# Kernel optimization log

Measured on AMD Instinct MI355X. Metric: run time of the kernel, lower is better.

The kernel has to match this reference:

```python
import jax, jax.numpy as jnp
import numpy as np

BATCH, SEQ, CH, ORDER = 4, 8192, 512, 64


def setup_inputs() -> dict:
    key = jax.random.key(0)
    k1, k2, k3 = jax.random.split(key, 3)
    x = jax.random.normal(k1, (BATCH, SEQ, CH), dtype=jnp.float32)
    # RTF parameters: small init so the denominator polynomial 1 + sum a_i z^-i
    # stays well-conditioned (stable transfer function), as in the FSSM init.
    A = 0.01 * jax.random.normal(k2, (CH, ORDER), dtype=jnp.float32)
    B = 0.01 * jax.random.normal(k3, (CH, ORDER), dtype=jnp.float32)
    h0 = jnp.zeros((1,), dtype=jnp.float32)
    return {"x": x, "A": A, "B": B, "h0": h0}


def _rtf_kernel(A, B, L):
    # Evaluate H(z) = b(z)/a(z) at the L roots of unity, then irfft -> impulse response.
    C = A.shape[0]
    a = jnp.concatenate([jnp.ones((C, 1), A.dtype), A], axis=-1)  # (C, N+1), leading coeff 1
    a_f = jnp.fft.rfft(a, n=L, axis=-1)                           # (C, L//2+1)
    b_f = jnp.fft.rfft(B, n=L, axis=-1)
    return jnp.fft.irfft(b_f / a_f, n=L, axis=-1)                 # (C, L)


def reference(x, A, B, h0):
    Bt, L, C = x.shape
    K = _rtf_kernel(A, B, L)                                      # (C, L)
    n_fft = 2 * L                                                 # causal (linear) convolution
    x_f = jnp.fft.rfft(x, n=n_fft, axis=1)                        # (B, n_fft//2+1, C)
    k_f = jnp.fft.rfft(K, n=n_fft, axis=-1).T[None]               # (1, n_fft//2+1, C)
    h1 = jnp.fft.irfft(x_f * k_f, n=n_fft, axis=1)[:, :L]         # (B, L, C)
    y1 = h1 + h0 * x
    return jax.nn.gelu(y1)
```

## Files before the change

### kernel.cpp

```cpp
#include <hip/hip_runtime.h>
#include <stdint.h>

#define NBATCH 4
#define LSEQ   8192
#define CH     512
#define ORDER  64
#define KTAP   256

typedef _Float16 half8 __attribute__((ext_vector_type(8)));
typedef _Float16 half4 __attribute__((ext_vector_type(4)));
typedef float    f32x4 __attribute__((ext_vector_type(4)));

#define PADP  8512
#define PAD0  279
#define NW    9

#define AFRAG_HALFS  ((size_t)CH * NW * 64 * 8)
#define XT_HALFS     ((size_t)CH * NBATCH * PADP)
#define WS_NEED      ((AFRAG_HALFS + XT_HALFS) * 2)

#define NAPREP 128
#define NXPOSE (133 * 8 * NBATCH)

__global__ __launch_bounds__(256) void prep(const float* __restrict__ A,
                                            const float* __restrict__ B,
                                            const float* __restrict__ h0,
                                            const float* __restrict__ x,
                                            _Float16* __restrict__ afr,
                                            _Float16* __restrict__ xT) {
    __shared__ float    Ksh[4][KTAP];
    __shared__ _Float16 tile[64][74];
    const int bid = blockIdx.x;
    if (bid < NAPREP) {
        const int wv = threadIdx.x >> 6, lane = threadIdx.x & 63;
        const int c  = bid * 4 + wv;
        const float a  = A[c * ORDER + lane];
        const float bc = B[c * ORDER + lane];
        const float h0v = h0[0];
        float s = 0.0f;
        for (int t = 0; t < KTAP; ++t) {
            const float s1 = __shfl(s, 0);
            const float bt = (t < ORDER) ? __shfl(bc, t) : 0.0f;
            const float y  = bt + s1;
            float su = __shfl_down(s, 1);
            if (lane == ORDER - 1) su = 0.0f;
            s = su - a * y;
            if (lane == 0) Ksh[wv][t] = (t == 0) ? (y + h0v) : y;
        }
        __syncthreads();
        const int i = lane & 15, g = lane >> 4;
        for (int w = 0; w < NW; ++w) {
            half8 hv;
#pragma unroll
            for (int e = 0; e < 8; ++e) {
                const int t = 32 * w + 15 + i - 8 * g - e;
                hv[e] = (_Float16)((t >= 0 && t < KTAP) ? Ksh[wv][t] : 0.0f);
            }
            *reinterpret_cast<half8*>(afr + ((size_t)(c * NW + w) * 64 + lane) * 8) = hv;
        }
    } else {
        const int bid2 = bid - NAPREP;
        const int px   = bid2 % 133;
        const int cy   = (bid2 / 133) & 7;
        const int bz   = bid2 / (133 * 8);
        const int p0 = px * 64, c0 = cy * 64, t = threadIdx.x;
        const int cl = (t & 15) * 4;
        const int rl = t >> 4;
#pragma unroll
        for (int pass = 0; pass < 4; ++pass) {
            const int pl = rl + 16 * pass;
            const int r  = p0 + pl - PAD0;
            float4 v = {0.0f, 0.0f, 0.0f, 0.0f};
            if (r >= 0 && r < LSEQ)
                v = *reinterpret_cast<const float4*>(x + ((size_t)bz * LSEQ + r) * CH + c0 + cl);
            tile[pl][cl + 0] = (_Float16)v.x;
            tile[pl][cl + 1] = (_Float16)v.y;
            tile[pl][cl + 2] = (_Float16)v.z;
            tile[pl][cl + 3] = (_Float16)v.w;
        }
        __syncthreads();
        const int pl2 = (t & 15) * 4;
#pragma unroll
        for (int pass = 0; pass < 4; ++pass) {
            const int cc = (t >> 4) + 16 * pass;
            half4 hv;
#pragma unroll
            for (int d = 0; d < 4; ++d) hv[d] = tile[pl2 + d][cc];
            *reinterpret_cast<half4*>(xT + ((size_t)((c0 + cc) * NBATCH + bz)) * PADP + p0 + pl2) = hv;
        }
    }
}

__global__ __launch_bounds__(256) void fir_mfma(const _Float16* __restrict__ xT,
                                                const _Float16* __restrict__ afr,
                                                float* __restrict__ out) {
    __shared__ _Float16 xs[16][1312];
    __shared__ float    lds_out[16][260];
    const int gid     = blockIdx.x;
    const int logical = (gid & 7) * 128 + (gid >> 3);
    const int chgrp   = logical >> 5;
    const int rem     = logical & 31;
    const int bb      = rem >> 3;
    const int tg      = rem & 7;

    {
        const int grp = threadIdx.x >> 4;
        const int l16 = threadIdx.x & 15;
        const size_t rowbase = ((size_t)(chgrp * 16 + grp) * NBATCH + bb) * PADP
                             + (size_t)tg * 1024 + 8;
#pragma unroll
        for (int it = 0; it < 11; ++it) {
            const int chunk = l16 + 16 * it;
            if (chunk < 164) {
                const half8 v = *reinterpret_cast<const half8*>(xT + rowbase + (size_t)chunk * 8);
                *reinterpret_cast<half8*>(&xs[grp][chunk * 8]) = v;
            }
        }
    }
    __syncthreads();

    const int wid = threadIdx.x >> 6, lane = threadIdx.x & 63;
    const int j = lane & 15, g = lane >> 4;
    const int c0 = chgrp * 16 + wid * 4;
    const _Float16* af = afr + (size_t)lane * 8;

    f32x4 acc[4][4];
#pragma unroll
    for (int ti = 0; ti < 4; ++ti)
#pragma unroll
        for (int q = 0; q < 4; ++q) acc[ti][q] = (f32x4){0.f, 0.f, 0.f, 0.f};

#pragma unroll
    for (int w = 0; w < NW; ++w) {
        half8 a[4];
#pragma unroll
        for (int q = 0; q < 4; ++q)
            a[q] = *reinterpret_cast<const half8*>(af + (size_t)((c0 + q) * NW + w) * 512);
        const int base = 16 * j + 8 * g - 32 * w + 256;
#pragma unroll
        for (int ti = 0; ti < 4; ++ti) {
#pragma unroll
            for (int q = 0; q < 4; ++q) {
                const half8 bv = *reinterpret_cast<const half8*>(&xs[wid * 4 + q][base + 256 * ti]);
                acc[ti][q] = __builtin_amdgcn_mfma_f32_16x16x32_f16(a[q], bv, acc[ti][q], 0, 0, 0);
            }
        }
    }

    const int ccs = threadIdx.x & 15, nb = threadIdx.x >> 4;
#pragma unroll
    for (int ti = 0; ti < 4; ++ti) {
        __syncthreads();
#pragma unroll
        for (int q = 0; q < 4; ++q) {
            f32x4 o;
#pragma unroll
            for (int r = 0; r < 4; ++r) {
                const float y  = acc[ti][q][r];
                const float m2 = y * y;
                const float wv = fmaf(m2, 0.14270963f, 1.5957691f);
                const float e  = __expf(y * wv);
                const float rc = __builtin_amdgcn_rcpf(e + 1.0f);
                o[r] = y - y * rc;
            }
            *reinterpret_cast<f32x4*>(&lds_out[wid * 4 + q][16 * j + 4 * g]) = o;
        }
        __syncthreads();
        const int n0 = tg * 1024 + ti * 256;
        float* ob = out + ((size_t)bb * LSEQ + n0) * CH + chgrp * 16 + ccs;
#pragma unroll
        for (int it = 0; it < 16; ++it) {
            const int nrel = nb + 16 * it;
            ob[(size_t)nrel * CH] = lds_out[ccs][nrel];
        }
    }
}

#define RINGF 32
#define CPBF  256
__global__ __launch_bounds__(ORDER) void rtf_impulse_fb(const float* __restrict__ A,
                                                        const float* __restrict__ B,
                                                        const float* __restrict__ h0,
                                                        float* __restrict__ kt4) {
    const int c = blockIdx.x, lane = threadIdx.x;
    const float a = A[c * ORDER + lane], bc = B[c * ORDER + lane], h0v = h0[0];
    float s = 0.0f;
    for (int t = 0; t < KTAP; ++t) {
        const float s1 = __shfl(s, 0);
        const float bt = (t < ORDER) ? __shfl(bc, t) : 0.0f;
        const float y  = bt + s1;
        float su = __shfl_down(s, 1);
        if (lane == ORDER - 1) su = 0.0f;
        s = su - a * y;
        if (lane == 0) kt4[((size_t)(t >> 2) * CH + c) * 4 + (t & 3)] = (t == 0) ? (y + h0v) : y;
    }
}
__global__ __launch_bounds__(CPBF) void fir_gelu_fb(const float* __restrict__ x,
                                                    const float* __restrict__ kt4,
                                                    float* __restrict__ out) {
    const int h = blockIdx.x;
    const int logical = ((h & 7) << 8) | (h >> 3);
    const int tile = logical & 255, sl = logical >> 8;
    const int cb = sl & 1, b = sl >> 1;
    const int c = cb * CPBF + threadIdx.x;
    const int n0 = tile * RINGF;
    const float* xb = x + (size_t)b * LSEQ * CH + c;
    const float4* kt4v = (const float4*)kt4;
    float acc[RINGF]; float ring[RINGF]; float px[2][8]; float kbuf[2][8];
#pragma unroll
    for (int r = 0; r < RINGF; ++r) acc[r] = 0.0f;
#pragma unroll
    for (int i = 0; i < RINGF; ++i) ring[i] = xb[(size_t)(n0 + i) * CH];
    {
        const float4 ka = kt4v[(size_t)0 * CH + c];
        const float4 kb = kt4v[(size_t)1 * CH + c];
        kbuf[0][0] = ka.x; kbuf[0][1] = ka.y; kbuf[0][2] = ka.z; kbuf[0][3] = ka.w;
        kbuf[0][4] = kb.x; kbuf[0][5] = kb.y; kbuf[0][6] = kb.z; kbuf[0][7] = kb.w;
#pragma unroll
        for (int g2 = 0; g2 < 8; ++g2) {
            const int m = n0 - 1 - g2;
            px[0][g2] = (m >= 0) ? xb[(size_t)m * CH] : 0.0f;
        }
    }
    for (int tb = 0; tb < KTAP; tb += RINGF) {
#pragma unroll
        for (int q = 0; q < 4; ++q) {
            const int cur = q & 1, nxt = cur ^ 1;
            const int tn = tb + 8 * (q + 1);
            if (tn < KTAP) {
                const float4 ka = kt4v[(size_t)(tn >> 2) * CH + c];
                const float4 kb = kt4v[(size_t)((tn >> 2) + 1) * CH + c];
                kbuf[nxt][0] = ka.x; kbuf[nxt][1] = ka.y; kbuf[nxt][2] = ka.z; kbuf[nxt][3] = ka.w;
                kbuf[nxt][4] = kb.x; kbuf[nxt][5] = kb.y; kbuf[nxt][6] = kb.z; kbuf[nxt][7] = kb.w;
#pragma unroll
                for (int g2 = 0; g2 < 8; ++g2) {
                    const int m = n0 - tn - 1 - g2;
                    px[nxt][g2] = (m >= 0) ? xb[(size_t)m * CH] : 0.0f;
                }
            }
#pragma unroll
            for (int g2 = 0; g2 < 8; ++g2) {
                const int tq = 8 * q + g2;
                const float kv = kbuf[cur][g2];
#pragma unroll
                for (int r = 0; r < RINGF; ++r)
                    acc[r] = fmaf(kv, ring[(r - tq) & (RINGF - 1)], acc[r]);
                ring[(RINGF - 1 - tq) & (RINGF - 1)] = px[cur][g2];
            }
        }
    }
    float* ob = out + ((size_t)b * LSEQ + n0) * CH + c;
#pragma unroll
    for (int r = 0; r < RINGF; ++r) {
        const float y = acc[r];
        const float m2 = y * y;
        const float wv = fmaf(m2, 0.14270963f, 1.5957691f);
        const float e = __expf(y * wv);
        const float rc = __builtin_amdgcn_rcpf(e + 1.0f);
        ob[(size_t)r * CH] = y - y * rc;
    }
}

extern "C" void kernel_launch(void* const* d_in, const int* in_sizes, int n_in,
                              void* d_out, int out_size, void* d_ws, size_t ws_size,
                              hipStream_t stream) {
    const float* x  = (const float*)d_in[0];
    const float* A  = (const float*)d_in[1];
    const float* B  = (const float*)d_in[2];
    const float* h0 = (const float*)d_in[3];
    float* out = (float*)d_out;

    if (ws_size >= WS_NEED) {
        _Float16* afr = (_Float16*)d_ws;
        _Float16* xT  = afr + AFRAG_HALFS;
        prep<<<dim3(NAPREP + NXPOSE), dim3(256), 0, stream>>>(A, B, h0, x, afr, xT);
        fir_mfma<<<dim3(1024), dim3(256), 0, stream>>>(xT, afr, out);
    } else {
        float* kt4 = (float*)d_ws;
        rtf_impulse_fb<<<dim3(CH), dim3(ORDER), 0, stream>>>(A, B, h0, kt4);
        fir_gelu_fb<<<dim3((LSEQ / RINGF) * (CH / CPBF) * NBATCH), dim3(CPBF), 0, stream>>>(x, kt4, out);
    }
}
```

Measured before the change: 60.74 us.

## Fuse x transpose/fp16 conversion into FIR kernel and vectorize output stores

```diff
diff --git a/kernel.cpp b/kernel.cpp
--- a/kernel.cpp
+++ b/kernel.cpp
@@ -8,112 +8,92 @@
 #define KTAP   256
 
 typedef _Float16 half8 __attribute__((ext_vector_type(8)));
-typedef _Float16 half4 __attribute__((ext_vector_type(4)));
+typedef _Float16 f16x2 __attribute__((ext_vector_type(2)));
 typedef float    f32x4 __attribute__((ext_vector_type(4)));
 
-#define PADP  8512
-#define PAD0  279
 #define NW    9
-
 #define AFRAG_HALFS  ((size_t)CH * NW * 64 * 8)
-#define XT_HALFS     ((size_t)CH * NBATCH * PADP)
-#define WS_NEED      ((AFRAG_HALFS + XT_HALFS) * 2)
-
-#define NAPREP 128
-#define NXPOSE (133 * 8 * NBATCH)
-
-__global__ __launch_bounds__(256) void prep(const float* __restrict__ A,
-                                            const float* __restrict__ B,
-                                            const float* __restrict__ h0,
-                                            const float* __restrict__ x,
-                                            _Float16* __restrict__ afr,
-                                            _Float16* __restrict__ xT) {
-    __shared__ float    Ksh[4][KTAP];
-    __shared__ _Float16 tile[64][74];
-    const int bid = blockIdx.x;
-    if (bid < NAPREP) {
-        const int wv = threadIdx.x >> 6, lane = threadIdx.x & 63;
-        const int c  = bid * 4 + wv;
-        const float a  = A[c * ORDER + lane];
-        const float bc = B[c * ORDER + lane];
-        const float h0v = h0[0];
-        float s = 0.0f;
-        for (int t = 0; t < KTAP; ++t) {
-            const float s1 = __shfl(s, 0);
-            const float bt = (t < ORDER) ? __shfl(bc, t) : 0.0f;
-            const float y  = bt + s1;
-            float su = __shfl_down(s, 1);
-            if (lane == ORDER - 1) su = 0.0f;
-            s = su - a * y;
-            if (lane == 0) Ksh[wv][t] = (t == 0) ? (y + h0v) : y;
-        }
-        __syncthreads();
-        const int i = lane & 15, g = lane >> 4;
-        for (int w = 0; w < NW; ++w) {
-            half8 hv;
-#pragma unroll
-            for (int e = 0; e < 8; ++e) {
-                const int t = 32 * w + 15 + i - 8 * g - e;
-                hv[e] = (_Float16)((t >= 0 && t < KTAP) ? Ksh[wv][t] : 0.0f);
-            }
-            *reinterpret_cast<half8*>(afr + ((size_t)(c * NW + w) * 64 + lane) * 8) = hv;
-        }
-    } else {
-        const int bid2 = bid - NAPREP;
-        const int px   = bid2 % 133;
-        const int cy   = (bid2 / 133) & 7;
-        const int bz   = bid2 / (133 * 8);
-        const int p0 = px * 64, c0 = cy * 64, t = threadIdx.x;
-        const int cl = (t & 15) * 4;
-        const int rl = t >> 4;
-#pragma unroll
-        for (int pass = 0; pass < 4; ++pass) {
-            const int pl = rl + 16 * pass;
-            const int r  = p0 + pl - PAD0;
-            float4 v = {0.0f, 0.0f, 0.0f, 0.0f};
-            if (r >= 0 && r < LSEQ)
-                v = *reinterpret_cast<const float4*>(x + ((size_t)bz * LSEQ + r) * CH + c0 + cl);
-            tile[pl][cl + 0] = (_Float16)v.x;
-            tile[pl][cl + 1] = (_Float16)v.y;
-            tile[pl][cl + 2] = (_Float16)v.z;
-            tile[pl][cl + 3] = (_Float16)v.w;
-        }
-        __syncthreads();
-        const int pl2 = (t & 15) * 4;
-#pragma unroll
-        for (int pass = 0; pass < 4; ++pass) {
-            const int cc = (t >> 4) + 16 * pass;
-            half4 hv;
-#pragma unroll
-            for (int d = 0; d < 4; ++d) hv[d] = tile[pl2 + d][cc];
-            *reinterpret_cast<half4*>(xT + ((size_t)((c0 + cc) * NBATCH + bz)) * PADP + p0 + pl2) = hv;
-        }
-    }
-}
-
-__global__ __launch_bounds__(256) void fir_mfma(const _Float16* __restrict__ xT,
+#define WS_NEED      (AFRAG_HALFS * 2)
+
+#define XSW   1320
+#define XROWB 2640
+#define LOW   260
+#define LOWB  1040
+#define SMEMB (16 * XROWB)
+
+__device__ __forceinline__ uint32_t packh2(_Float16 lo, _Float16 hi) {
+    f16x2 v; v.x = lo; v.y = hi;
+    return __builtin_bit_cast(uint32_t, v);
+}
+
+__global__ __launch_bounds__(256) void rtf_afrag(const float* __restrict__ A,
+                                                 const float* __restrict__ B,
+                                                 const float* __restrict__ h0,
+                                                 _Float16* __restrict__ afr) {
+    __shared__ float Ksh[4][KTAP];
+    const int wv = threadIdx.x >> 6, lane = threadIdx.x & 63;
+    const int c  = blockIdx.x * 4 + wv;
+    const float a  = A[c * ORDER + lane];
+    const float bc = B[c * ORDER + lane];
+    const float h0v = h0[0];
+    float s = 0.0f;
+    for (int t = 0; t < KTAP; ++t) {
+        const float s1 = __shfl(s, 0);
+        const float bt = (t < ORDER) ? __shfl(bc, t) : 0.0f;
+        const float y  = bt + s1;
+        float su = __shfl_down(s, 1);
+        if (lane == ORDER - 1) su = 0.0f;
+        s = su - a * y;
+        if (lane == 0) Ksh[wv][t] = (t == 0) ? (y + h0v) : y;
+    }
+    __syncthreads();
+    const int i = lane & 15, g = lane >> 4;
+    for (int w = 0; w < NW; ++w) {
+        half8 hv;
+#pragma unroll
+        for (int e = 0; e < 8; ++e) {
+            const int t = 32 * w + 15 + i - 8 * g - e;
+            hv[e] = (_Float16)((t >= 0 && t < KTAP) ? Ksh[wv][t] : 0.0f);
+        }
+        *reinterpret_cast<half8*>(afr + ((size_t)(c * NW + w) * 64 + lane) * 8) = hv;
+    }
+}
+
+__global__ __launch_bounds__(256) void fir_mfma(const float* __restrict__ x,
                                                 const _Float16* __restrict__ afr,
                                                 float* __restrict__ out) {
-    __shared__ _Float16 xs[16][1312];
-    __shared__ float    lds_out[16][260];
+    __shared__ __align__(16) char smem[SMEMB];
     const int gid     = blockIdx.x;
     const int logical = (gid & 7) * 128 + (gid >> 3);
     const int chgrp   = logical >> 5;
     const int rem     = logical & 31;
     const int bb      = rem >> 3;
     const int tg      = rem & 7;
+    const int n0      = tg * 1024;
 
     {
-        const int grp = threadIdx.x >> 4;
-        const int l16 = threadIdx.x & 15;
-        const size_t rowbase = ((size_t)(chgrp * 16 + grp) * NBATCH + bb) * PADP
-                             + (size_t)tg * 1024 + 8;
+        const int cg = threadIdx.x & 3;
+        const int pr = threadIdx.x >> 2;
+        const float* xsrc = x + (size_t)bb * LSEQ * CH + chgrp * 16 + cg * 4;
 #pragma unroll
         for (int it = 0; it < 11; ++it) {
-            const int chunk = l16 + 16 * it;
-            if (chunk < 164) {
-                const half8 v = *reinterpret_cast<const half8*>(xT + rowbase + (size_t)chunk * 8);
-                *reinterpret_cast<half8*>(&xs[grp][chunk * 8]) = v;
+            const int p = pr + 64 * it;
+            if (p < 656) {
+                const int r0 = n0 - 271 + 2 * p;
+                float4 v0 = {0.f, 0.f, 0.f, 0.f}, v1 = v0;
+                if (r0 >= 0 && r0 < LSEQ)
+                    v0 = *reinterpret_cast<const float4*>(xsrc + (size_t)r0 * CH);
+                if (r0 + 1 >= 0 && r0 + 1 < LSEQ)
+                    v1 = *reinterpret_cast<const float4*>(xsrc + (size_t)(r0 + 1) * CH);
+                char* base = smem + (size_t)(cg * 4) * XROWB + 4 * p;
+                *reinterpret_cast<uint32_t*>(base + 0 * XROWB) =
+                    packh2((_Float16)v0.x, (_Float16)v1.x);
+                *reinterpret_cast<uint32_t*>(base + 1 * XROWB) =
+                    packh2((_Float16)v0.y, (_Float16)v1.y);
+                *reinterpret_cast<uint32_t*>(base + 2 * XROWB) =
+                    packh2((_Float16)v0.z, (_Float16)v1.z);
+                *reinterpret_cast<uint32_t*>(base + 3 * XROWB) =
+                    packh2((_Float16)v0.w, (_Float16)v1.w);
             }
         }
     }
@@ -141,13 +121,15 @@
         for (int ti = 0; ti < 4; ++ti) {
 #pragma unroll
             for (int q = 0; q < 4; ++q) {
-                const half8 bv = *reinterpret_cast<const half8*>(&xs[wid * 4 + q][base + 256 * ti]);
+                const half8 bv = *reinterpret_cast<const half8*>(
+                    smem + (size_t)(wid * 4 + q) * XROWB + 2 * (base + 256 * ti));
                 acc[ti][q] = __builtin_amdgcn_mfma_f32_16x16x32_f16(a[q], bv, acc[ti][q], 0, 0, 0);
             }
         }
     }
 
-    const int ccs = threadIdx.x & 15, nb = threadIdx.x >> 4;
+    const int cq = threadIdx.x & 3;
+    const int nq = threadIdx.x >> 2;
 #pragma unroll
     for (int ti = 0; ti < 4; ++ti) {
         __syncthreads();
@@ -163,15 +145,20 @@
                 const float rc = __builtin_amdgcn_rcpf(e + 1.0f);
                 o[r] = y - y * rc;
             }
-            *reinterpret_cast<f32x4*>(&lds_out[wid * 4 + q][16 * j + 4 * g]) = o;
+            *reinterpret_cast<f32x4*>(smem + (size_t)(wid * 4 + q) * LOWB
+                                      + 4 * (16 * j + 4 * g)) = o;
         }
         __syncthreads();
-        const int n0 = tg * 1024 + ti * 256;
-        float* ob = out + ((size_t)bb * LSEQ + n0) * CH + chgrp * 16 + ccs;
-#pragma unroll
-        for (int it = 0; it < 16; ++it) {
-            const int nrel = nb + 16 * it;
-            ob[(size_t)nrel * CH] = lds_out[ccs][nrel];
+        float* ob = out + ((size_t)bb * LSEQ + n0 + ti * 256) * CH + chgrp * 16 + cq * 4;
+#pragma unroll
+        for (int it = 0; it < 4; ++it) {
+            const int n = nq + 64 * it;
+            float4 o;
+            o.x = *reinterpret_cast<float*>(smem + (size_t)(cq * 4 + 0) * LOWB + 4 * n);
+            o.y = *reinterpret_cast<float*>(smem + (size_t)(cq * 4 + 1) * LOWB + 4 * n);
+            o.z = *reinterpret_cast<float*>(smem + (size_t)(cq * 4 + 2) * LOWB + 4 * n);
+            o.w = *reinterpret_cast<float*>(smem + (size_t)(cq * 4 + 3) * LOWB + 4 * n);
+            *reinterpret_cast<float4*>(ob + (size_t)n * CH) = o;
         }
     }
 }
@@ -272,9 +259,8 @@
 
     if (ws_size >= WS_NEED) {
         _Float16* afr = (_Float16*)d_ws;
-        _Float16* xT  = afr + AFRAG_HALFS;
-        prep<<<dim3(NAPREP + NXPOSE), dim3(256), 0, stream>>>(A, B, h0, x, afr, xT);
-        fir_mfma<<<dim3(1024), dim3(256), 0, stream>>>(xT, afr, out);
+        rtf_afrag<<<dim3(CH / 4), dim3(256), 0, stream>>>(A, B, h0, afr);
+        fir_mfma<<<dim3(1024), dim3(256), 0, stream>>>(x, afr, out);
     } else {
         float* kt4 = (float*)d_ws;
         rtf_impulse_fb<<<dim3(CH), dim3(ORDER), 0, stream>>>(A, B, h0, kt4);
```

After: 63.79 us. +5.0%, slower.
